# Performance work log

Measured on AMD Instinct MI355X. Metric: run time of the kernel, lower is better.

## Reference

```python
import jax, jax.numpy as jnp
import numpy as np

BIT_SIZE = 8
ES_SIZE = 1
IN_F = 2048
OUT_F = 2048
N = 8192


def posit_quantize(x, nbits, es):
    """Round-to-nearest posit(nbits, es) quantization, returned as float32.

    Posit value: sign * useed^k * 2^e * (1+f), useed = 2^(2^es).
    Regime length rlen = k+2 (k>=0) or -k+1 (k<0); fraction bits =
    nbits - 1(sign) - rlen - es, clamped at 0. Magnitudes are clamped to
    [minpos, maxpos] (posits never round a nonzero value to zero/inf).
    """
    two_es = 2 ** es                      # useed = 2**two_es
    npat = nbits - 2
    maxpos = jnp.float32(2.0 ** (two_es * npat))
    minpos = jnp.float32(2.0 ** (-two_es * npat))

    sign = jnp.sign(x)
    ax = jnp.clip(jnp.abs(x), minpos, maxpos)

    s = jnp.floor(jnp.log2(ax))           # integer power-of-two scale
    k = jnp.floor(s / two_es)             # regime value
    rlen = jnp.where(k >= 0, k + 2.0, -k + 1.0)
    fbits = jnp.maximum(nbits - 1.0 - rlen - es, 0.0)

    m = ax * jnp.exp2(-s)                 # mantissa in [1, 2)
    fscale = jnp.exp2(fbits)
    mq = jnp.round(m * fscale) / fscale   # round fraction to fbits
    # carry: mantissa rounded up to 2.0 -> bump exponent
    s = jnp.where(mq >= 2.0, s + 1.0, s)
    mq = jnp.where(mq >= 2.0, 1.0, mq)

    y = sign * mq * jnp.exp2(s)
    y = jnp.clip(y, -maxpos, maxpos)
    return jnp.where(x == 0, jnp.float32(0.0), y).astype(x.dtype)


def setup_inputs() -> dict:
    key = jax.random.key(0)
    kx, kw, kb = jax.random.split(key, 3)
    x = jax.random.normal(kx, (N, IN_F), dtype=jnp.float32)
    bound = 1.0 / np.sqrt(IN_F)  # nn.Linear default init range
    weight = jax.random.uniform(kw, (OUT_F, IN_F), dtype=jnp.float32,
                                minval=-bound, maxval=bound)
    bias = jax.random.uniform(kb, (OUT_F,), dtype=jnp.float32,
                              minval=-bound, maxval=bound)
    return {"x": x, "weight": weight, "bias": bias}


def reference(x, weight, bias):
    xq = posit_quantize(x, BIT_SIZE, ES_SIZE)
    wq = posit_quantize(weight, BIT_SIZE, ES_SIZE)
    bq = posit_quantize(bias, BIT_SIZE, ES_SIZE)
    # y = xq @ wq^T + bq  (nn.Linear)
    return jnp.einsum('ni,oi->no', xq, wq) + bq
```

## Files before the change

### kernel.cpp

```cpp
#include <hip/hip_runtime.h>

typedef __attribute__((ext_vector_type(8))) short bf16x8;
typedef __attribute__((ext_vector_type(4))) float f32x4;

__device__ __forceinline__ float posit_q(float x) {
  float ax = fabsf(x);
  ax = fmaxf(ax, 0x1p-12f);
  ax = fminf(ax, 0x1p12f);
  int s = (int)(__float_as_uint(ax) >> 23) - 127;
  int k = s >> 1;
  int rlen = (k >= 0) ? (k + 2) : (1 - k);
  int fbits = 6 - rlen;
  fbits = fbits < 0 ? 0 : fbits;
  float m = ax * __uint_as_float((unsigned)(127 - s) << 23);
  float fs = (float)(1 << fbits);
  float inv_fs = __uint_as_float((unsigned)(127 - fbits) << 23);
  float mq = rintf(m * fs) * inv_fs;
  if (mq >= 2.0f) { s += 1; mq = 1.0f; }
  float y = mq * __uint_as_float((unsigned)(127 + s) << 23);
  y = fminf(y, 0x1p12f);
  y = copysignf(y, x);
  return (x == 0.0f) ? 0.0f : y;
}

__global__ void posit_quant_bf16(const float* __restrict__ in,
                                 ushort* __restrict__ out, int n4) {
  int i = blockIdx.x * blockDim.x + threadIdx.x;
  int stride = gridDim.x * blockDim.x;
  for (; i < n4; i += stride) {
    float4 v = ((const float4*)in)[i];
    ushort4 o;
    o.x = (ushort)(__float_as_uint(posit_q(v.x)) >> 16);
    o.y = (ushort)(__float_as_uint(posit_q(v.y)) >> 16);
    o.z = (ushort)(__float_as_uint(posit_q(v.z)) >> 16);
    o.w = (ushort)(__float_as_uint(posit_q(v.w)) >> 16);
    ((ushort4*)out)[i] = o;
  }
}

__global__ void posit_quant_f32(const float* __restrict__ in,
                                float* __restrict__ out, int n) {
  int i = blockIdx.x * blockDim.x + threadIdx.x;
  if (i < n) out[i] = posit_q(in[i]);
}

__device__ __forceinline__ void gl_lds16(const ushort* g, ushort* l) {
  __builtin_amdgcn_global_load_lds(
      (const __attribute__((address_space(1))) void*)g,
      (__attribute__((address_space(3))) void*)l,
      16, 0, 0);
}

__global__ __launch_bounds__(256, 2) void posit_gemm(
    const ushort* __restrict__ A, const ushort* __restrict__ B,
    const float* __restrict__ bq, float* __restrict__ C,
    int M, int N, int K) {
  __shared__ ushort sA[128 * 32];
  __shared__ ushort sB[128 * 32];

  const int tid = threadIdx.x;
  const int wave = tid >> 6;
  const int lane = tid & 63;
  const int wm = wave >> 1;
  const int wn = wave & 1;
  const int m0 = blockIdx.y << 7;
  const int n0 = blockIdx.x << 7;

  const int c0 = (wave << 6) + lane;
  const int r0 = c0 >> 2;
  const int q0 = (c0 & 3) << 3;
  const int r1 = r0 + 64;

  const ushort* Ag0 = A + (size_t)(m0 + r0) * K + q0;
  const ushort* Ag1 = A + (size_t)(m0 + r1) * K + q0;
  const ushort* Bg0 = B + (size_t)(n0 + r0) * K + q0;
  const ushort* Bg1 = B + (size_t)(n0 + r1) * K + q0;

  ushort* lA0 = sA + (wave << 9);
  ushort* lA1 = sA + 2048 + (wave << 9);
  ushort* lB0 = sB + (wave << 9);
  ushort* lB1 = sB + 2048 + (wave << 9);

  const int fr = lane & 15;
  const int fk = (lane >> 4) << 3;

  f32x4 acc[4][4];
#pragma unroll
  for (int i = 0; i < 4; i++)
#pragma unroll
    for (int j = 0; j < 4; j++) acc[i][j] = (f32x4){0.f, 0.f, 0.f, 0.f};

  for (int k0 = 0; k0 < K; k0 += 32) {
    gl_lds16(Ag0 + k0, lA0);
    gl_lds16(Ag1 + k0, lA1);
    gl_lds16(Bg0 + k0, lB0);
    gl_lds16(Bg1 + k0, lB1);
    __syncthreads();

    bf16x8 fa[4], fb[4];
#pragma unroll
    for (int i = 0; i < 4; i++)
      fa[i] = *(const bf16x8*)(sA + (((wm << 6) + (i << 4) + fr) << 5) + fk);
#pragma unroll
    for (int j = 0; j < 4; j++)
      fb[j] = *(const bf16x8*)(sB + (((wn << 6) + (j << 4) + fr) << 5) + fk);

#pragma unroll
    for (int i = 0; i < 4; i++)
#pragma unroll
      for (int j = 0; j < 4; j++)
        acc[i][j] = __builtin_amdgcn_mfma_f32_16x16x32_bf16(
            fa[i], fb[j], acc[i][j], 0, 0, 0);
    __syncthreads();
  }

  const int row0 = m0 + (wm << 6) + ((lane >> 4) << 2);
  const int col0 = n0 + (wn << 6) + fr;
#pragma unroll
  for (int j = 0; j < 4; j++) {
    const int col = col0 + (j << 4);
    const float bv = bq[col];
#pragma unroll
    for (int i = 0; i < 4; i++) {
      const int row = row0 + (i << 4);
#pragma unroll
      for (int r = 0; r < 4; r++)
        C[(size_t)(row + r) * N + col] = acc[i][j][r] + bv;
    }
  }
}

extern "C" void kernel_launch(void* const* d_in, const int* in_sizes, int n_in,
                              void* d_out, int out_size, void* d_ws, size_t ws_size,
                              hipStream_t stream) {
  const float* x = (const float*)d_in[0];
  const float* w = (const float*)d_in[1];
  const float* bias = (const float*)d_in[2];
  float* out = (float*)d_out;

  const int out_f = in_sizes[2];
  const int in_f = in_sizes[1] / out_f;
  const int m = in_sizes[0] / in_f;
  const int k = in_f;

  ushort* Xq = (ushort*)d_ws;
  ushort* Wq = Xq + (size_t)m * k;
  float* bquant = (float*)(Wq + (size_t)out_f * k);

  {
    int n4 = in_sizes[0] / 4;
    int blocks = (n4 + 255) / 256;
    if (blocks > 16384) blocks = 16384;
    posit_quant_bf16<<<blocks, 256, 0, stream>>>(x, Xq, n4);
  }
  {
    int n4 = in_sizes[1] / 4;
    int blocks = (n4 + 255) / 256;
    if (blocks > 16384) blocks = 16384;
    posit_quant_bf16<<<blocks, 256, 0, stream>>>(w, Wq, n4);
  }
  posit_quant_f32<<<(out_f + 255) / 256, 256, 0, stream>>>(bias, bquant, out_f);

  dim3 grid(out_f / 128, m / 128);
  posit_gemm<<<grid, 256, 0, stream>>>(Xq, Wq, bquant, out, m, out_f, k);
}
```

Baseline: 211.7 us.

## Fuse posit quantization kernels and XOR-swizzle LDS tiles to avoid bank conflicts

Replaces the three separate quantization launches (x, weight, bias) with a single kernel covering all three ranges, removing two launch overheads. In the GEMM, the global-to-LDS load permutes each row's 16-byte k-chunk by an XOR of row bits, and the fragment reads use the matching swizzled offset. The goal is to cut LDS bank conflicts on the bf16x8 fragment loads. The fused kernel drops the grid-stride cap and adds a branch per thread, and the bias path now assumes the bias length is a multiple of four.

```diff
diff --git a/kernel.cpp b/kernel.cpp
--- a/kernel.cpp
+++ b/kernel.cpp
@@ -23,25 +23,36 @@
   return (x == 0.0f) ? 0.0f : y;
 }
 
-__global__ void posit_quant_bf16(const float* __restrict__ in,
-                                 ushort* __restrict__ out, int n4) {
-  int i = blockIdx.x * blockDim.x + threadIdx.x;
-  int stride = gridDim.x * blockDim.x;
-  for (; i < n4; i += stride) {
-    float4 v = ((const float4*)in)[i];
-    ushort4 o;
-    o.x = (ushort)(__float_as_uint(posit_q(v.x)) >> 16);
-    o.y = (ushort)(__float_as_uint(posit_q(v.y)) >> 16);
-    o.z = (ushort)(__float_as_uint(posit_q(v.z)) >> 16);
-    o.w = (ushort)(__float_as_uint(posit_q(v.w)) >> 16);
-    ((ushort4*)out)[i] = o;
-  }
+__device__ __forceinline__ ushort4 quant4_bf16(float4 v) {
+  ushort4 o;
+  o.x = (ushort)(__float_as_uint(posit_q(v.x)) >> 16);
+  o.y = (ushort)(__float_as_uint(posit_q(v.y)) >> 16);
+  o.z = (ushort)(__float_as_uint(posit_q(v.z)) >> 16);
+  o.w = (ushort)(__float_as_uint(posit_q(v.w)) >> 16);
+  return o;
 }
 
-__global__ void posit_quant_f32(const float* __restrict__ in,
-                                float* __restrict__ out, int n) {
+__global__ void posit_quant_all(const float* __restrict__ x,
+                                const float* __restrict__ w,
+                                const float* __restrict__ b,
+                                ushort* __restrict__ Xq,
+                                ushort* __restrict__ Wq,
+                                float* __restrict__ bq,
+                                int nx4, int nw4, int nb4) {
   int i = blockIdx.x * blockDim.x + threadIdx.x;
-  if (i < n) out[i] = posit_q(in[i]);
+  if (i < nx4) {
+    ((ushort4*)Xq)[i] = quant4_bf16(((const float4*)x)[i]);
+  } else if (i < nx4 + nw4) {
+    int j = i - nx4;
+    ((ushort4*)Wq)[j] = quant4_bf16(((const float4*)w)[j]);
+  } else if (i < nx4 + nw4 + nb4) {
+    int j = i - nx4 - nw4;
+    float4 v = ((const float4*)b)[j];
+    float4 o;
+    o.x = posit_q(v.x); o.y = posit_q(v.y);
+    o.z = posit_q(v.z); o.w = posit_q(v.w);
+    ((float4*)bq)[j] = o;
+  }
 }
 
 __device__ __forceinline__ void gl_lds16(const ushort* g, ushort* l) {
@@ -68,7 +79,8 @@
 
   const int c0 = (wave << 6) + lane;
   const int r0 = c0 >> 2;
-  const int q0 = (c0 & 3) << 3;
+  const int p0 = c0 & 3;
+  const int q0 = ((p0 ^ ((r0 >> 1) & 3)) << 3);
   const int r1 = r0 + 64;
 
   const ushort* Ag0 = A + (size_t)(m0 + r0) * K + q0;
@@ -82,7 +94,7 @@
   ushort* lB1 = sB + 2048 + (wave << 9);
 
   const int fr = lane & 15;
-  const int fk = (lane >> 4) << 3;
+  const int fkp = (((lane >> 4) ^ ((fr >> 1) & 3)) << 3);
 
   f32x4 acc[4][4];
 #pragma unroll
@@ -100,10 +112,10 @@
     bf16x8 fa[4], fb[4];
 #pragma unroll
     for (int i = 0; i < 4; i++)
-      fa[i] = *(const bf16x8*)(sA + (((wm << 6) + (i << 4) + fr) << 5) + fk);
+      fa[i] = *(const bf16x8*)(sA + (((wm << 6) + (i << 4) + fr) << 5) + fkp);
 #pragma unroll
     for (int j = 0; j < 4; j++)
-      fb[j] = *(const bf16x8*)(sB + (((wn << 6) + (j << 4) + fr) << 5) + fk);
+      fb[j] = *(const bf16x8*)(sB + (((wn << 6) + (j << 4) + fr) << 5) + fkp);
 
 #pragma unroll
     for (int i = 0; i < 4; i++)
@@ -147,19 +159,12 @@
   ushort* Wq = Xq + (size_t)m * k;
   float* bquant = (float*)(Wq + (size_t)out_f * k);
 
-  {
-    int n4 = in_sizes[0] / 4;
-    int blocks = (n4 + 255) / 256;
-    if (blocks > 16384) blocks = 16384;
-    posit_quant_bf16<<<blocks, 256, 0, stream>>>(x, Xq, n4);
-  }
-  {
-    int n4 = in_sizes[1] / 4;
-    int blocks = (n4 + 255) / 256;
-    if (blocks > 16384) blocks = 16384;
-    posit_quant_bf16<<<blocks, 256, 0, stream>>>(w, Wq, n4);
-  }
-  posit_quant_f32<<<(out_f + 255) / 256, 256, 0, stream>>>(bias, bquant, out_f);
+  const int nx4 = in_sizes[0] / 4;
+  const int nw4 = in_sizes[1] / 4;
+  const int nb4 = in_sizes[2] / 4;
+  const int total4 = nx4 + nw4 + nb4;
+  posit_quant_all<<<(total4 + 255) / 256, 256, 0, stream>>>(
+      x, w, bias, Xq, Wq, bquant, nx4, nw4, nb4);
 
   dim3 grid(out_f / 128, m / 128);
   posit_gemm<<<grid, 256, 0, stream>>>(Xq, Wq, bquant, out, m, out_f, k);
```

Result: faster. 205.9 us (-2.8%).
